# Kernel tuning notes

Hardware: AMD Instinct MI355X
Metric: run time of the kernel (lower is better)

## Reference

```python
import jax, jax.numpy as jnp
import numpy as np

TOP_K = 400
IGNORE = 255


def setup_inputs() -> dict:
    key = jax.random.key(0)
    k = jax.random.split(key, 6)
    B, C, H, W = 16, 3, 768, 768
    D, He, We = 64, 192, 192
    return {
        "outputs": jax.random.normal(k[0], (B, C, H, W), jnp.float32),
        "embeddings": jax.random.normal(k[1], (B, D, He, We), jnp.float32),
        "class_labels": jax.random.randint(k[2], (B, H, W), 0, 3, jnp.int32),
        "outputs_aug": jax.random.normal(k[3], (B, C, H, W), jnp.float32),
        "embeddings_aug": jax.random.normal(k[4], (B, D, He, We), jnp.float32),
        "class_labels_aug": jax.random.randint(k[5], (B, H, W), 0, 3, jnp.int32),
    }


def _nearest_down(x, He, We):
    # torch F.interpolate(mode='nearest') with integer downscale factor == strided slice
    sH = x.shape[-2] // He
    sW = x.shape[-1] // We
    return x[..., ::sH, ::sW]


def _forward(outputs, embeddings, outputs_aug, embeddings_aug, class_labels):
    B, C, H, W = outputs.shape
    D, He, We = embeddings.shape[1], embeddings.shape[2], embeddings.shape[3]

    # --- CrossEntropy(ignore_index=255), per-sample mean, averaged over batch ---
    logp = jax.nn.log_softmax(outputs, axis=1)                      # [B,C,H,W]
    valid = class_labels != IGNORE                                   # [B,H,W]
    lbl = jnp.where(valid, class_labels, 0).astype(jnp.int32)
    nll = -jnp.take_along_axis(logp, lbl[:, None], axis=1)[:, 0]     # [B,H,W]
    loss_ce = ((nll * valid).sum((1, 2)) / jnp.maximum(valid.sum((1, 2)), 1)).mean()

    # --- confidence / prediction maps, downsampled to embedding resolution ---
    def conf_seg(o):
        p = jax.nn.softmax(o, axis=1)
        return p.max(axis=1), p.argmax(axis=1)

    conf, seg = conf_seg(outputs)
    conf_a, seg_a = conf_seg(outputs_aug)
    segd = _nearest_down(seg, He, We)
    confd = _nearest_down(conf, He, We)
    segd_a = _nearest_down(seg_a, He, We)
    confd_a = _nearest_down(conf_a, He, We)

    def per_sample(emb, emb_a, sg, cf, sg_a, cf_a):
        ef = emb.reshape(D, -1)                                      # [D,P]
        efa = emb_a.reshape(D, -1)
        n = ef / jnp.linalg.norm(ef, axis=0, keepdims=True)          # unit columns
        na = efa / jnp.linalg.norm(efa, axis=0, keepdims=True)
        sgf, cff = sg.ravel(), cf.ravel()
        sgfa, cffa = sg_a.ravel(), cf_a.ravel()

        # ---- class 1 (ths=0.8): sort masked pixels by channel-mean, take top_k ----
        m1 = (sgf == 1) & (cff > 0.8)
        m1a = (sgfa == 1) & (cffa > 0.8)

        def topk_sel(nrm, ef_, m):
            keyv = jnp.where(m, ef_.mean(0), jnp.inf)  # unmasked -> +inf, sorted last
            idx = jnp.argsort(keyv)[:TOP_K]
            return nrm[:, idx]                         # [D,TOP_K], already unit-norm

        s1 = topk_sel(n, ef, m1)
        s1a = topk_sel(na, efa, m1a)
        d1 = 1.0 - (s1.T @ s1a).mean()                 # mean pairwise cosine distance
        v1 = (m1.sum() > TOP_K) & (m1a.sum() > TOP_K)

        # ---- class 2 (ths=0.6): all masked pixels; mean over pairs of cos-sim
        # equals dot of masked means of unit vectors (exact identity) ----
        m2 = (sgf == 2) & (cff > 0.6)
        m2a = (sgfa == 2) & (cffa > 0.6)
        mu = (n * m2).sum(1) / jnp.maximum(m2.sum(), 1)
        mua = (na * m2a).sum(1) / jnp.maximum(m2a.sum(), 1)
        d2 = 1.0 - mu @ mua
        v2 = (m2.sum() > 0) & (m2a.sum() > 0)
        return d1, v1, d2, v2

    d1, v1, d2, v2 = jax.vmap(per_sample)(embeddings, embeddings_aug, segd, confd, segd_a, confd_a)
    cnt = v1.sum() + v2.sum()
    loss_matching = (jnp.where(v1, d1, 0.0).sum() + jnp.where(v2, d2, 0.0).sum()) / jnp.maximum(cnt, 1)
    loss = loss_ce + 2.0 * loss_matching
    return loss, loss_ce, loss_matching


def reference(outputs, embeddings, class_labels, outputs_aug, embeddings_aug, class_labels_aug):
    # class_labels_aug does not enter the loss in the original code (aug CE is built but never added)
    return _forward(outputs, embeddings, outputs_aug, embeddings_aug, class_labels)
```

## Files before the change

### kernel.cpp

```cpp
#include <hip/hip_runtime.h>
#include <cstdint>
#include <cstddef>

#define Bn 16
#define Cn 3
#define Hn 768
#define Wn 768
#define Dn 64
#define HEn 192
#define WEn 192
#define Pn (HEn * WEn)
#define HWn (Hn * Wn)
#define TOPK 400
#define SENTK 0xFFFFFFFFu
#define PAD 16

struct Ws {
  float ce_sum[Bn][PAD];
  int   ce_cnt[Bn][PAD];
  int   cnt1[2][Bn][PAD];
  int   cnt2[2][Bn][PAD];
  float mu2[2][Bn][Dn][PAD];
  float mu1[2][Bn][Dn][PAD];
  int   nsel[2][Bn];
  int   idxl[2][Bn][TOPK];
  unsigned keys[2][Bn][Pn];
};
#define INIT_WORDS (256 + 256 + 512 + 512 + 32768 + 32768)
static_assert(offsetof(Ws, nsel) == (size_t)INIT_WORDS * 4, "ws layout");
static_assert(sizeof(Ws) < (size_t)6 * 1024 * 1024, "ws small");

__global__ void init_kernel(Ws* ws) {
  unsigned* w = (unsigned*)ws;
  int t = blockIdx.x * blockDim.x + threadIdx.x;
  for (int i = t; i < INIT_WORDS; i += gridDim.x * blockDim.x) w[i] = 0u;
}

__device__ __forceinline__ float wave_sum_f(float s) {
#pragma unroll
  for (int off = 32; off; off >>= 1) s += __shfl_down(s, off);
  return s;
}
__device__ __forceinline__ int wave_sum_i(int s) {
#pragma unroll
  for (int off = 32; off; off >>= 1) s += __shfl_down(s, off);
  return s;
}

__global__ void ce_kernel(const float* __restrict__ out, const int* __restrict__ lab,
                          Ws* __restrict__ ws) {
  int b = blockIdx.y;
  const int NT = 72 * 256;
  int t = blockIdx.x * 256 + threadIdx.x;
  const float* base = out + (size_t)b * Cn * HWn;
  const int* lb_base = lab + (size_t)b * HWn;
  float s = 0.f; int c = 0;
#pragma unroll
  for (int it = 0; it < 8; it++) {
    int p4 = (t + it * NT) * 4;
    float4 a0 = *(const float4*)(base + p4);
    float4 a1 = *(const float4*)(base + HWn + p4);
    float4 a2 = *(const float4*)(base + 2 * HWn + p4);
    int4 lb = *(const int4*)(lb_base + p4);
    float x0s[4] = {a0.x, a0.y, a0.z, a0.w};
    float x1s[4] = {a1.x, a1.y, a1.z, a1.w};
    float x2s[4] = {a2.x, a2.y, a2.z, a2.w};
    int ls[4] = {lb.x, lb.y, lb.z, lb.w};
#pragma unroll
    for (int k = 0; k < 4; k++) {
      int l = ls[k];
      if (l != 255) {
        float x0 = x0s[k], x1 = x1s[k], x2 = x2s[k];
        float m = fmaxf(x0, fmaxf(x1, x2));
        float lse = m + __logf(__expf(x0 - m) + __expf(x1 - m) + __expf(x2 - m));
        float xl = (l == 0) ? x0 : ((l == 1) ? x1 : x2);
        s += lse - xl;
        c += 1;
      }
    }
  }
  s = wave_sum_f(s);
  c = wave_sum_i(c);
  __shared__ float ss[4];
  __shared__ int sc[4];
  int wid = threadIdx.x >> 6;
  if ((threadIdx.x & 63) == 0) { ss[wid] = s; sc[wid] = c; }
  __syncthreads();
  if (threadIdx.x == 0) {
    atomicAdd(&ws->ce_sum[b][0], ss[0] + ss[1] + ss[2] + ss[3]);
    atomicAdd(&ws->ce_cnt[b][0], sc[0] + sc[1] + sc[2] + sc[3]);
  }
}

__global__ void main_kernel(const float* __restrict__ o0, const float* __restrict__ o1,
                            const float* __restrict__ e0, const float* __restrict__ e1,
                            Ws* __restrict__ ws) {
  int arr = blockIdx.z;
  int b = blockIdx.y;
  int p = blockIdx.x * blockDim.x + threadIdx.x;
  int lane = threadIdx.x & 63, wid = threadIdx.x >> 6;
  const float* o = (arr ? o1 : o0) + (size_t)b * Cn * HWn;
  int i = p / WEn, j = p - i * WEn;
  int q = (4 * i) * Wn + 4 * j;
  float x0 = o[q], x1 = o[q + HWn], x2 = o[q + 2 * HWn];
  int s = 0; float m = x0;
  if (x1 > m) { m = x1; s = 1; }
  if (x2 > m) { m = x2; s = 2; }
  float conf = 1.0f / (__expf(x0 - m) + __expf(x1 - m) + __expf(x2 - m));
  bool m1 = (s == 1) && (conf > 0.8f);
  bool m2 = (s == 2) && (conf > 0.6f);

  const float* e = (arr ? e1 : e0) + (size_t)b * Dn * Pn + p;
  float v[Dn];
  float sum = 0.f, sq = 0.f;
#pragma unroll
  for (int d = 0; d < Dn; d++) {
    float x = e[(size_t)d * Pn];
    v[d] = x; sum += x; sq += x * x;
  }
  unsigned kb = SENTK;
  if (m1) {
    unsigned u = __float_as_uint(sum);
    kb = (u & 0x80000000u) ? ~u : (u | 0x80000000u);
    if (kb == SENTK) kb--;
  }
  ws->keys[arr][b][p] = kb;

  __shared__ int scnt1[4], scnt2[4];
  unsigned long long bal1 = __ballot(m1), bal2 = __ballot(m2);
  if (lane == 0) { scnt1[wid] = (int)__popcll(bal1); scnt2[wid] = (int)__popcll(bal2); }

  float rn = m2 ? rsqrtf(sq) : 0.f;
  __shared__ float red[4 * Dn];
  float mine = 0.f;
#pragma unroll
  for (int d = 0; d < Dn; d++) {
    float x = v[d] * rn;
#pragma unroll
    for (int off = 1; off < 64; off <<= 1) x += __shfl_xor(x, off);
    if (lane == d) mine = x;
  }
  red[wid * Dn + lane] = mine;
  __syncthreads();
  if (threadIdx.x < Dn) {
    float S = red[threadIdx.x] + red[Dn + threadIdx.x] +
              red[2 * Dn + threadIdx.x] + red[3 * Dn + threadIdx.x];
    if (S != 0.f) atomicAdd(&ws->mu2[arr][b][threadIdx.x][0], S);
  }
  if (threadIdx.x == 0) {
    int c1 = scnt1[0] + scnt1[1] + scnt1[2] + scnt1[3];
    int c2 = scnt2[0] + scnt2[1] + scnt2[2] + scnt2[3];
    if (c1) atomicAdd(&ws->cnt1[arr][b][0], c1);
    if (c2) atomicAdd(&ws->cnt2[arr][b][0], c2);
  }
}

__global__ void __launch_bounds__(1024) select_kernel(Ws* __restrict__ ws) {
  int arr = blockIdx.x >> 4;
  int b = blockIdx.x & 15;
  int tid = threadIdx.x;
  const unsigned* __restrict__ keys = ws->keys[arr][b];
  int c1 = ws->cnt1[arr][b][0];
  if (c1 <= TOPK) {
    if (tid == 0) ws->nsel[arr][b] = 0;
    return;
  }
  __shared__ int hist[2048];
  __shared__ int super[128];
  __shared__ int tieBuf[256];
  __shared__ unsigned sPrefix;
  __shared__ int sKRem, nBelow, nTie;
  if (tid == 0) { sPrefix = 0u; sKRem = TOPK; }

  const int shifts[3] = {21, 10, 0};
  const unsigned bmask[3] = {2047u, 2047u, 1023u};
  const int nbins[3] = {2048, 2048, 1024};

  for (int lvl = 0; lvl < 3; lvl++) {
    hist[tid] = 0;
    hist[tid + 1024] = 0;
    __syncthreads();
    unsigned pref = sPrefix;
    int shift = shifts[lvl];
    unsigned bm = bmask[lvl];
    for (int base = tid; base < Pn; base += 4096) {
      unsigned u0 = keys[base];
      unsigned u1 = keys[base + 1024];
      unsigned u2 = keys[base + 2048];
      unsigned u3 = keys[base + 3072];
#pragma unroll
      for (int k = 0; k < 4; k++) {
        unsigned u = (k == 0) ? u0 : (k == 1) ? u1 : (k == 2) ? u2 : u3;
        if (u == SENTK) continue;
        if (lvl == 1 && (u >> 21) != (pref >> 21)) continue;
        if (lvl == 2 && (u >> 10) != (pref >> 10)) continue;
        atomicAdd(&hist[(u >> shift) & bm], 1);
      }
    }
    __syncthreads();
    int SB = nbins[lvl] >> 7;
    if (tid < 128) {
      int s = 0;
      for (int k = 0; k < SB; k++) s += hist[tid * SB + k];
      super[tid] = s;
    }
    __syncthreads();
    if (tid == 0) {
      int k = sKRem, cum = 0, sb = 127;
      for (int t = 0; t < 128; t++) {
        if (cum + super[t] >= k) { sb = t; break; }
        cum += super[t];
      }
      int j = sb * SB + SB - 1;
      for (int t = sb * SB; t < sb * SB + SB; t++) {
        if (cum + hist[t] >= k) { j = t; k -= cum; break; }
        cum += hist[t];
      }
      sKRem = k;
      sPrefix = pref | ((unsigned)j << shift);
    }
    __syncthreads();
  }
  unsigned T = sPrefix;
  int kRem = sKRem;
  if (tid == 0) { nBelow = 0; nTie = 0; }
  __syncthreads();
  int* idxl = ws->idxl[arr][b];
  for (int base = tid; base < Pn; base += 4096) {
    unsigned u0 = keys[base];
    unsigned u1 = keys[base + 1024];
    unsigned u2 = keys[base + 2048];
    unsigned u3 = keys[base + 3072];
#pragma unroll
    for (int k = 0; k < 4; k++) {
      unsigned u = (k == 0) ? u0 : (k == 1) ? u1 : (k == 2) ? u2 : u3;
      int p = base + k * 1024;
      if (u < T) {
        int pos = atomicAdd(&nBelow, 1);
        if (pos < TOPK) idxl[pos] = p;
      } else if (u == T) {
        int tp = atomicAdd(&nTie, 1);
        if (tp < 256) tieBuf[tp] = p;
      }
    }
  }
  __syncthreads();
  if (tid == 0) {
    int nb = nBelow;
    int tn = nTie < 256 ? nTie : 256;
    int take = kRem < tn ? kRem : tn;
    for (int r = 0; r < take; r++) {
      int mi = r;
      for (int t = r + 1; t < tn; t++)
        if (tieBuf[t] < tieBuf[mi]) mi = t;
      int tmp = tieBuf[r]; tieBuf[r] = tieBuf[mi]; tieBuf[mi] = tmp;
      if (nb + r < TOPK) idxl[nb + r] = tieBuf[r];
    }
    int ns = nb + take;
    ws->nsel[arr][b] = ns > TOPK ? TOPK : ns;
  }
}

__global__ void accum1_kernel(const float* __restrict__ e0, const float* __restrict__ e1,
                              Ws* __restrict__ ws) {
  int arr = blockIdx.x >> 4;
  int b = blockIdx.x & 15;
  int ns = ws->nsel[arr][b];
  if (ns == 0) return;
  int lane = threadIdx.x & 63, wid = threadIdx.x >> 6;
  const float* e = (arr ? e1 : e0) + (size_t)b * Dn * Pn;
  float acc[Dn];
#pragma unroll
  for (int d = 0; d < Dn; d++) acc[d] = 0.f;
  for (int t = threadIdx.x; t < ns; t += blockDim.x) {
    int p = ws->idxl[arr][b][t];
    float v[Dn];
    float sq = 0.f;
#pragma unroll
    for (int d = 0; d < Dn; d++) {
      float x = e[(size_t)d * Pn + p];
      v[d] = x; sq += x * x;
    }
    float rn = rsqrtf(sq);
#pragma unroll
    for (int d = 0; d < Dn; d++) acc[d] += v[d] * rn;
  }
  __shared__ float red[4 * Dn];
  float mine = 0.f;
#pragma unroll
  for (int d = 0; d < Dn; d++) {
    float x = acc[d];
#pragma unroll
    for (int off = 1; off < 64; off <<= 1) x += __shfl_xor(x, off);
    if (lane == d) mine = x;
  }
  red[wid * Dn + lane] = mine;
  __syncthreads();
  if (threadIdx.x < Dn) {
    float S = red[threadIdx.x] + red[Dn + threadIdx.x] +
              red[2 * Dn + threadIdx.x] + red[3 * Dn + threadIdx.x];
    atomicAdd(&ws->mu1[arr][b][threadIdx.x][0], S);
  }
}

__global__ void final_kernel(Ws* __restrict__ ws, float* __restrict__ out) {
  int t = threadIdx.x;
  float ce = 0.f, num = 0.f;
  int cnt = 0;
  if (t < Bn) {
    int cc = ws->ce_cnt[t][0];
    ce = ws->ce_sum[t][0] / (float)(cc > 1 ? cc : 1);
    int c1o = ws->cnt1[0][t][0], c1a = ws->cnt1[1][t][0];
    if (c1o > TOPK && c1a > TOPK) {
      float dot = 0.f;
      for (int d = 0; d < Dn; d++) dot += ws->mu1[0][t][d][0] * ws->mu1[1][t][d][0];
      num += 1.f - dot / ((float)TOPK * (float)TOPK);
      cnt += 1;
    }
    int c2o = ws->cnt2[0][t][0], c2a = ws->cnt2[1][t][0];
    if (c2o > 0 && c2a > 0) {
      float dot = 0.f;
      for (int d = 0; d < Dn; d++) dot += ws->mu2[0][t][d][0] * ws->mu2[1][t][d][0];
      float den = (float)(c2o > 1 ? c2o : 1) * (float)(c2a > 1 ? c2a : 1);
      num += 1.f - dot / den;
      cnt += 1;
    }
  }
#pragma unroll
  for (int off = 32; off; off >>= 1) {
    ce += __shfl_down(ce, off);
    num += __shfl_down(num, off);
    cnt += __shfl_down(cnt, off);
  }
  if (t == 0) {
    float loss_ce = ce / (float)Bn;
    float lm = num / (float)(cnt > 1 ? cnt : 1);
    out[0] = loss_ce + 2.f * lm;
    out[1] = loss_ce;
    out[2] = lm;
  }
}

extern "C" void kernel_launch(void* const* d_in, const int* in_sizes, int n_in,
                              void* d_out, int out_size, void* d_ws, size_t ws_size,
                              hipStream_t stream) {
  const float* outputs      = (const float*)d_in[0];
  const float* embeddings   = (const float*)d_in[1];
  const int*   class_labels = (const int*)d_in[2];
  const float* outputs_aug  = (const float*)d_in[3];
  const float* emb_aug      = (const float*)d_in[4];
  Ws* ws = (Ws*)d_ws;
  float* out = (float*)d_out;

  init_kernel<<<32, 256, 0, stream>>>(ws);
  ce_kernel<<<dim3(72, Bn), 256, 0, stream>>>(outputs, class_labels, ws);
  main_kernel<<<dim3(Pn / 256, Bn, 2), 256, 0, stream>>>(outputs, outputs_aug,
                                                         embeddings, emb_aug, ws);
  select_kernel<<<32, 1024, 0, stream>>>(ws);
  accum1_kernel<<<32, 256, 0, stream>>>(embeddings, emb_aug, ws);
  final_kernel<<<1, 64, 0, stream>>>(ws, out);
}
```

Baseline: 591.3 us.

## Split embedding channels across waves and widen loads in main, select, accum kernels

The main kernel now assigns each wave 16 of the 64 embedding channels for 128 pixels, reading them with float2 loads. Per-pixel sums and sums of squares are combined through shared memory, which cuts register pressure from the 64-float per-thread array and shortens the shuffle-reduction chains. The select kernel reads keys as uint4, which changes the pixel-to-thread mapping. accum1 is spread over a 7x32 grid with the same channel split, and the CE kernel uses twice as many blocks with half the iterations. The cost is extra shared-memory syncs and more atomics into mu1 and mu2.

```diff
diff --git a/kernel.cpp b/kernel.cpp
--- a/kernel.cpp
+++ b/kernel.cpp
@@ -14,6 +14,7 @@
 #define TOPK 400
 #define SENTK 0xFFFFFFFFu
 #define PAD 16
+#define PXB 128
 
 struct Ws {
   float ce_sum[Bn][PAD];
@@ -50,13 +51,13 @@
 __global__ void ce_kernel(const float* __restrict__ out, const int* __restrict__ lab,
                           Ws* __restrict__ ws) {
   int b = blockIdx.y;
-  const int NT = 72 * 256;
+  const int NT = 144 * 256;
   int t = blockIdx.x * 256 + threadIdx.x;
   const float* base = out + (size_t)b * Cn * HWn;
   const int* lb_base = lab + (size_t)b * HWn;
   float s = 0.f; int c = 0;
 #pragma unroll
-  for (int it = 0; it < 8; it++) {
+  for (int it = 0; it < 4; it++) {
     int p4 = (t + it * NT) * 4;
     float4 a0 = *(const float4*)(base + p4);
     float4 a1 = *(const float4*)(base + HWn + p4);
@@ -97,69 +98,86 @@
                             Ws* __restrict__ ws) {
   int arr = blockIdx.z;
   int b = blockIdx.y;
-  int p = blockIdx.x * blockDim.x + threadIdx.x;
-  int lane = threadIdx.x & 63, wid = threadIdx.x >> 6;
-  const float* o = (arr ? o1 : o0) + (size_t)b * Cn * HWn;
-  int i = p / WEn, j = p - i * WEn;
-  int q = (4 * i) * Wn + 4 * j;
-  float x0 = o[q], x1 = o[q + HWn], x2 = o[q + 2 * HWn];
-  int s = 0; float m = x0;
-  if (x1 > m) { m = x1; s = 1; }
-  if (x2 > m) { m = x2; s = 2; }
-  float conf = 1.0f / (__expf(x0 - m) + __expf(x1 - m) + __expf(x2 - m));
-  bool m1 = (s == 1) && (conf > 0.8f);
-  bool m2 = (s == 2) && (conf > 0.6f);
-
-  const float* e = (arr ? e1 : e0) + (size_t)b * Dn * Pn + p;
-  float v[Dn];
-  float sum = 0.f, sq = 0.f;
-#pragma unroll
-  for (int d = 0; d < Dn; d++) {
-    float x = e[(size_t)d * Pn];
-    v[d] = x; sum += x; sq += x * x;
-  }
-  unsigned kb = SENTK;
-  if (m1) {
-    unsigned u = __float_as_uint(sum);
-    kb = (u & 0x80000000u) ? ~u : (u | 0x80000000u);
-    if (kb == SENTK) kb--;
-  }
-  ws->keys[arr][b][p] = kb;
-
-  __shared__ int scnt1[4], scnt2[4];
-  unsigned long long bal1 = __ballot(m1), bal2 = __ballot(m2);
-  if (lane == 0) { scnt1[wid] = (int)__popcll(bal1); scnt2[wid] = (int)__popcll(bal2); }
-
-  float rn = m2 ? rsqrtf(sq) : 0.f;
-  __shared__ float red[4 * Dn];
-  float mine = 0.f;
-#pragma unroll
-  for (int d = 0; d < Dn; d++) {
-    float x = v[d] * rn;
+  int lane = threadIdx.x & 63, wv = threadIdx.x >> 6;
+  int p0 = blockIdx.x * PXB;
+  int pa = p0 + 2 * lane;
+
+  const float* e = (arr ? e1 : e0) + ((size_t)b * Dn + wv * 16) * Pn;
+  float va[16], vb[16];
+  float sum0 = 0.f, sum1 = 0.f, sq0 = 0.f, sq1 = 0.f;
+#pragma unroll
+  for (int k = 0; k < 16; k++) {
+    float2 x = *(const float2*)(e + (size_t)k * Pn + pa);
+    va[k] = x.x; vb[k] = x.y;
+    sum0 += x.x; sq0 += x.x * x.x;
+    sum1 += x.y; sq1 += x.y * x.y;
+  }
+
+  __shared__ float psum[4][PXB], psq[4][PXB];
+  __shared__ float sscale[PXB];
+  *(float2*)&psum[wv][2 * lane] = make_float2(sum0, sum1);
+  *(float2*)&psq[wv][2 * lane] = make_float2(sq0, sq1);
+  __syncthreads();
+
+  if (wv == 0) {
+    const float* o = (arr ? o1 : o0) + (size_t)b * Cn * HWn;
+    unsigned kb[2]; float sc[2]; bool m1f[2], m2f[2];
+#pragma unroll
+    for (int h = 0; h < 2; h++) {
+      int px = 2 * lane + h;
+      int p = p0 + px;
+      float ts = psum[0][px] + psum[1][px] + psum[2][px] + psum[3][px];
+      float tq = psq[0][px] + psq[1][px] + psq[2][px] + psq[3][px];
+      int i = p / WEn, j = p - i * WEn;
+      int q = (4 * i) * Wn + 4 * j;
+      float x0 = o[q], x1 = o[q + HWn], x2 = o[q + 2 * HWn];
+      int sgc = 0; float m = x0;
+      if (x1 > m) { m = x1; sgc = 1; }
+      if (x2 > m) { m = x2; sgc = 2; }
+      float conf = 1.0f / (__expf(x0 - m) + __expf(x1 - m) + __expf(x2 - m));
+      bool m1 = (sgc == 1) && (conf > 0.8f);
+      bool m2 = (sgc == 2) && (conf > 0.6f);
+      unsigned kbv = SENTK;
+      if (m1) {
+        unsigned u = __float_as_uint(ts);
+        kbv = (u & 0x80000000u) ? ~u : (u | 0x80000000u);
+        if (kbv == SENTK) kbv--;
+      }
+      kb[h] = kbv;
+      sc[h] = m2 ? rsqrtf(tq) : 0.f;
+      m1f[h] = m1; m2f[h] = m2;
+    }
+    *(uint2*)&ws->keys[arr][b][pa] = make_uint2(kb[0], kb[1]);
+    *(float2*)&sscale[2 * lane] = make_float2(sc[0], sc[1]);
+    unsigned long long b10 = __ballot(m1f[0]), b11 = __ballot(m1f[1]);
+    unsigned long long b20 = __ballot(m2f[0]), b21 = __ballot(m2f[1]);
+    if (lane == 0) {
+      int c1 = (int)__popcll(b10) + (int)__popcll(b11);
+      int c2 = (int)__popcll(b20) + (int)__popcll(b21);
+      if (c1) atomicAdd(&ws->cnt1[arr][b][0], c1);
+      if (c2) atomicAdd(&ws->cnt2[arr][b][0], c2);
+    }
+  }
+  __syncthreads();
+
+  float2 s2 = *(const float2*)&sscale[2 * lane];
+  float rv = 0.f;
+#pragma unroll
+  for (int k = 0; k < 16; k++) {
+    float x = va[k] * s2.x + vb[k] * s2.y;
 #pragma unroll
     for (int off = 1; off < 64; off <<= 1) x += __shfl_xor(x, off);
-    if (lane == d) mine = x;
-  }
-  red[wid * Dn + lane] = mine;
-  __syncthreads();
-  if (threadIdx.x < Dn) {
-    float S = red[threadIdx.x] + red[Dn + threadIdx.x] +
-              red[2 * Dn + threadIdx.x] + red[3 * Dn + threadIdx.x];
-    if (S != 0.f) atomicAdd(&ws->mu2[arr][b][threadIdx.x][0], S);
-  }
-  if (threadIdx.x == 0) {
-    int c1 = scnt1[0] + scnt1[1] + scnt1[2] + scnt1[3];
-    int c2 = scnt2[0] + scnt2[1] + scnt2[2] + scnt2[3];
-    if (c1) atomicAdd(&ws->cnt1[arr][b][0], c1);
-    if (c2) atomicAdd(&ws->cnt2[arr][b][0], c2);
-  }
+    if (lane == k) rv = x;
+  }
+  if (lane < 16 && rv != 0.f)
+    atomicAdd(&ws->mu2[arr][b][wv * 16 + lane][0], rv);
 }
 
 __global__ void __launch_bounds__(1024) select_kernel(Ws* __restrict__ ws) {
   int arr = blockIdx.x >> 4;
   int b = blockIdx.x & 15;
   int tid = threadIdx.x;
-  const unsigned* __restrict__ keys = ws->keys[arr][b];
+  const uint4* __restrict__ keys4 = (const uint4*)ws->keys[arr][b];
   int c1 = ws->cnt1[arr][b][0];
   if (c1 <= TOPK) {
     if (tid == 0) ws->nsel[arr][b] = 0;
@@ -183,14 +201,13 @@
     unsigned pref = sPrefix;
     int shift = shifts[lvl];
     unsigned bm = bmask[lvl];
-    for (int base = tid; base < Pn; base += 4096) {
-      unsigned u0 = keys[base];
-      unsigned u1 = keys[base + 1024];
-      unsigned u2 = keys[base + 2048];
-      unsigned u3 = keys[base + 3072];
+#pragma unroll
+    for (int it = 0; it < 9; it++) {
+      uint4 u4 = keys4[it * 1024 + tid];
+      unsigned us[4] = {u4.x, u4.y, u4.z, u4.w};
 #pragma unroll
       for (int k = 0; k < 4; k++) {
-        unsigned u = (k == 0) ? u0 : (k == 1) ? u1 : (k == 2) ? u2 : u3;
+        unsigned u = us[k];
         if (u == SENTK) continue;
         if (lvl == 1 && (u >> 21) != (pref >> 21)) continue;
         if (lvl == 2 && (u >> 10) != (pref >> 10)) continue;
@@ -226,15 +243,14 @@
   if (tid == 0) { nBelow = 0; nTie = 0; }
   __syncthreads();
   int* idxl = ws->idxl[arr][b];
-  for (int base = tid; base < Pn; base += 4096) {
-    unsigned u0 = keys[base];
-    unsigned u1 = keys[base + 1024];
-    unsigned u2 = keys[base + 2048];
-    unsigned u3 = keys[base + 3072];
+#pragma unroll
+  for (int it = 0; it < 9; it++) {
+    uint4 u4 = keys4[it * 1024 + tid];
+    unsigned us[4] = {u4.x, u4.y, u4.z, u4.w};
 #pragma unroll
     for (int k = 0; k < 4; k++) {
-      unsigned u = (k == 0) ? u0 : (k == 1) ? u1 : (k == 2) ? u2 : u3;
-      int p = base + k * 1024;
+      unsigned u = us[k];
+      int p = (it * 1024 + tid) * 4 + k;
       if (u < T) {
         int pos = atomicAdd(&nBelow, 1);
         if (pos < TOPK) idxl[pos] = p;
@@ -263,44 +279,37 @@
 
 __global__ void accum1_kernel(const float* __restrict__ e0, const float* __restrict__ e1,
                               Ws* __restrict__ ws) {
-  int arr = blockIdx.x >> 4;
-  int b = blockIdx.x & 15;
+  int arr = blockIdx.y >> 4;
+  int b = blockIdx.y & 15;
+  int chunk = blockIdx.x;
   int ns = ws->nsel[arr][b];
-  if (ns == 0) return;
-  int lane = threadIdx.x & 63, wid = threadIdx.x >> 6;
-  const float* e = (arr ? e1 : e0) + (size_t)b * Dn * Pn;
-  float acc[Dn];
-#pragma unroll
-  for (int d = 0; d < Dn; d++) acc[d] = 0.f;
-  for (int t = threadIdx.x; t < ns; t += blockDim.x) {
-    int p = ws->idxl[arr][b][t];
-    float v[Dn];
-    float sq = 0.f;
-#pragma unroll
-    for (int d = 0; d < Dn; d++) {
-      float x = e[(size_t)d * Pn + p];
-      v[d] = x; sq += x * x;
-    }
-    float rn = rsqrtf(sq);
-#pragma unroll
-    for (int d = 0; d < Dn; d++) acc[d] += v[d] * rn;
-  }
-  __shared__ float red[4 * Dn];
-  float mine = 0.f;
-#pragma unroll
-  for (int d = 0; d < Dn; d++) {
-    float x = acc[d];
+  if (chunk * 64 >= ns) return;
+  int lane = threadIdx.x & 63, wv = threadIdx.x >> 6;
+  int t = chunk * 64 + lane;
+  bool valid = t < ns;
+  int p = valid ? ws->idxl[arr][b][t] : 0;
+  const float* e = (arr ? e1 : e0) + ((size_t)b * Dn + wv * 16) * Pn;
+  float v[16]; float sq = 0.f;
+#pragma unroll
+  for (int k = 0; k < 16; k++) {
+    float x = e[(size_t)k * Pn + p];
+    v[k] = x; sq += x * x;
+  }
+  __shared__ float psq[4][64];
+  psq[wv][lane] = sq;
+  __syncthreads();
+  float tq = psq[0][lane] + psq[1][lane] + psq[2][lane] + psq[3][lane];
+  float s = valid ? rsqrtf(tq) : 0.f;
+  float rv = 0.f;
+#pragma unroll
+  for (int k = 0; k < 16; k++) {
+    float x = v[k] * s;
 #pragma unroll
     for (int off = 1; off < 64; off <<= 1) x += __shfl_xor(x, off);
-    if (lane == d) mine = x;
-  }
-  red[wid * Dn + lane] = mine;
-  __syncthreads();
-  if (threadIdx.x < Dn) {
-    float S = red[threadIdx.x] + red[Dn + threadIdx.x] +
-              red[2 * Dn + threadIdx.x] + red[3 * Dn + threadIdx.x];
-    atomicAdd(&ws->mu1[arr][b][threadIdx.x][0], S);
-  }
+    if (lane == k) rv = x;
+  }
+  if (lane < 16 && rv != 0.f)
+    atomicAdd(&ws->mu1[arr][b][wv * 16 + lane][0], rv);
 }
 
 __global__ void final_kernel(Ws* __restrict__ ws, float* __restrict__ out) {
@@ -353,10 +362,10 @@
   float* out = (float*)d_out;
 
   init_kernel<<<32, 256, 0, stream>>>(ws);
-  ce_kernel<<<dim3(72, Bn), 256, 0, stream>>>(outputs, class_labels, ws);
-  main_kernel<<<dim3(Pn / 256, Bn, 2), 256, 0, stream>>>(outputs, outputs_aug,
+  ce_kernel<<<dim3(144, Bn), 256, 0, stream>>>(outputs, class_labels, ws);
+  main_kernel<<<dim3(Pn / PXB, Bn, 2), 256, 0, stream>>>(outputs, outputs_aug,
                                                          embeddings, emb_aug, ws);
   select_kernel<<<32, 1024, 0, stream>>>(ws);
-  accum1_kernel<<<32, 256, 0, stream>>>(embeddings, emb_aug, ws);
+  accum1_kernel<<<dim3(7, 32), 256, 0, stream>>>(embeddings, emb_aug, ws);
   final_kernel<<<1, 64, 0, stream>>>(ws, out);
 }
```

After: 530.1 us. 10.4% less time.
